# Optimization experiments

Hardware: AMD Instinct MI355X
Metric: run time of the kernel (lower is better)

## Reference

```python
import jax, jax.numpy as jnp
import numpy as np

H = 1152; NH = 16; HD = 72; INTER = 4304; DEPTH = 4
C = 3; T = 2; P = 16; G = 48; M = 2; S = G * G
MERGED = H * M * M; OUT = 2048; ROT = HD // 2  # rotary_pos_emb_dim = head_dim//2


def _ln(x, w, b, eps=1e-6):
    # manual LayerNorm decomposition (mean/var/rsqrt), fp32 like the original
    m = x.mean(-1, keepdims=True)
    xc = x - m
    v = (xc * xc).mean(-1, keepdims=True)
    return w * (xc * jax.lax.rsqrt(v + eps)) + b


def _gelu(x):
    return jax.nn.gelu(x, approximate=True)  # tanh approximation


def _rot_half(x):
    h = x.shape[-1] // 2
    return jnp.concatenate([-x[..., h:], x[..., :h]], axis=-1)


def _pos_ids():
    # Qwen merge-pattern token order: 2x2 spatial blocks are contiguous
    ids = np.arange(G * G).reshape(G // M, M, G // M, M).transpose(0, 2, 1, 3).reshape(-1)
    return jnp.asarray(ids, dtype=jnp.int32)


def setup_inputs() -> dict:
    key = jax.random.key(0)
    ks = jax.random.split(key, 16)
    w = lambda k, shape: jax.random.normal(k, shape, jnp.float32) * 0.02
    return {
        'pixel_values': jax.random.normal(ks[0], (S, C * T * P * P), jnp.float32),
        'cu_seqlens': jnp.array([0, S], jnp.int32),
        'conv_w': w(ks[1], (H, C, T, P, P)),
        'conv_b': jnp.zeros((H,), jnp.float32),
        'pos_tab': w(ks[2], (G * G, H)),
        'ln1_w': jnp.ones((DEPTH, H), jnp.float32), 'ln1_b': jnp.zeros((DEPTH, H), jnp.float32),
        'ln2_w': jnp.ones((DEPTH, H), jnp.float32), 'ln2_b': jnp.zeros((DEPTH, H), jnp.float32),
        'qkv_w': w(ks[3], (DEPTH, 3 * H, H)), 'qkv_b': jnp.zeros((DEPTH, 3 * H), jnp.float32),
        'proj_w': w(ks[4], (DEPTH, H, H)), 'proj_b': jnp.zeros((DEPTH, H), jnp.float32),
        'fc1_w': w(ks[5], (DEPTH, INTER, H)), 'fc1_b': jnp.zeros((DEPTH, INTER), jnp.float32),
        'fc2_w': w(ks[6], (DEPTH, H, INTER)), 'fc2_b': jnp.zeros((DEPTH, H), jnp.float32),
        'm_norm_w': jnp.ones((H,), jnp.float32), 'm_norm_b': jnp.zeros((H,), jnp.float32),
        'm_fc1_w': w(ks[7], (MERGED, MERGED)), 'm_fc1_b': jnp.zeros((MERGED,), jnp.float32),
        'm_fc2_w': w(ks[8], (OUT, MERGED)), 'm_fc2_b': jnp.zeros((OUT,), jnp.float32),
    }


def reference(pixel_values, cu_seqlens, conv_w, conv_b, pos_tab,
              ln1_w, ln1_b, ln2_w, ln2_b, qkv_w, qkv_b, proj_w, proj_b,
              fc1_w, fc1_b, fc2_w, fc2_b, m_norm_w, m_norm_b,
              m_fc1_w, m_fc1_b, m_fc2_w, m_fc2_b):
    pos_ids = _pos_ids()
    # Conv3d with stride == kernel over pre-extracted patches == matmul
    x = pixel_values @ conv_w.reshape(H, -1).T + conv_b            # [S, H]
    x = x + pos_tab[pos_ids]
    # 2D rotary: h-freqs and w-freqs each ROT/2 dims, concat -> ROT, dup -> HD
    inv_freq = 1.0 / (10000.0 ** (jnp.arange(0, ROT, 2, dtype=jnp.float32) / ROT))
    hp = (pos_ids // G).astype(jnp.float32)
    wp = (pos_ids % G).astype(jnp.float32)
    freqs = jnp.concatenate([hp[:, None] * inv_freq, wp[:, None] * inv_freq], axis=-1)  # [S, ROT]
    emb = jnp.concatenate([freqs, freqs], axis=-1)                 # [S, HD]
    cos = jnp.cos(emb)[:, None, :]                                 # [S, 1, HD]
    sin = jnp.sin(emb)[:, None, :]
    # varlen attention: block-diagonal mask from cu_seqlens
    seg = jnp.searchsorted(cu_seqlens, jnp.arange(S), side='right')
    mask = jnp.where(seg[:, None] == seg[None, :], 0.0, -1e9).astype(jnp.float32)
    scale = 1.0 / np.sqrt(HD)
    for i in range(DEPTH):
        h = _ln(x, ln1_w[i], ln1_b[i])
        qkv = (h @ qkv_w[i].T + qkv_b[i]).reshape(S, 3, NH, HD)
        q, k, v = qkv[:, 0], qkv[:, 1], qkv[:, 2]
        q = q * cos + _rot_half(q) * sin
        k = k * cos + _rot_half(k) * sin
        scores = jnp.einsum('qhd,khd->hqk', q, k) * scale + mask
        attn = jax.nn.softmax(scores, axis=-1)
        o = jnp.einsum('hqk,khd->qhd', attn, v).reshape(S, H)
        x = x + o @ proj_w[i].T + proj_b[i]
        h2 = _ln(x, ln2_w[i], ln2_b[i])
        x = x + _gelu(h2 @ fc1_w[i].T + fc1_b[i]) @ fc2_w[i].T + fc2_b[i]
    # patch merger: pre-merge LN -> reshape to merged -> fc1 -> gelu(tanh) -> fc2
    y = _ln(x, m_norm_w, m_norm_b).reshape(-1, MERGED)             # [S/4, MERGED]
    return _gelu(y @ m_fc1_w.T + m_fc1_b) @ m_fc2_w.T + m_fc2_b   # [S/4, OUT]
```

## Files before the change

### kernel.cpp

```cpp
#include <hip/hip_runtime.h>
#include <hip/hip_bf16.h>
#include <math.h>

#define S 2304
#define HDIM 1152
#define NHEAD 16
#define HD 72
#define INTER 4304
#define INTERP 4352
#define DEPTH 4
#define MERGED 4608
#define OUTD 2048
#define KIN 1536
#define NSPLIT 2
#define KHALF (S / NSPLIT)

typedef float f4 __attribute__((ext_vector_type(4)));
typedef short s8v __attribute__((ext_vector_type(8)));

__device__ __forceinline__ int pos_id_of(int s) {
  int a = s / 96;
  int r = s % 96;
  int b = r >> 2;
  int c = (r >> 1) & 1;
  int d = r & 1;
  return a * 96 + c * 48 + b * 2 + d;
}

__device__ __forceinline__ float gelu_f(float v) {
  const float c = 0.7978845608028654f;
  float t = tanhf(c * (v + 0.044715f * v * v * v));
  return 0.5f * v * (1.f + t);
}

__device__ __forceinline__ unsigned short f2b(float f) {
  unsigned int u = __float_as_uint(f);
  u += 0x7fffu + ((u >> 16) & 1u);
  return (unsigned short)(u >> 16);
}
__device__ __forceinline__ float b2f(unsigned short u) {
  return __uint_as_float(((unsigned int)u) << 16);
}

__device__ __forceinline__ void gload16(const void* g, void* l) {
  __builtin_amdgcn_global_load_lds(
      (const __attribute__((address_space(1))) void*)g,
      (__attribute__((address_space(3))) void*)l, 16, 0, 0);
}

__device__ __forceinline__ int xcd_swz(int flat, int nwg) {
  int q = nwg >> 3, r8 = nwg & 7;
  int xcd = flat & 7, lin = flat >> 3;
  return (xcd < r8 ? xcd * (q + 1) : r8 * (q + 1) + (xcd - r8) * q) + lin;
}

__global__ void __launch_bounds__(256) cvt_kernel(
    const float* __restrict__ src, unsigned short* __restrict__ dst,
    int N, int Ksrc, int Kdst)
{
  int idx = blockIdx.x * 256 + threadIdx.x;
  int kc = Kdst >> 3;
  if (idx >= N * kc) return;
  int r = idx / kc;
  int c8 = (idx % kc) << 3;
  const float* sp = src + (size_t)r * Ksrc + c8;
  unsigned short outv[8];
#pragma unroll
  for (int e = 0; e < 8; ++e)
    outv[e] = (c8 + e < Ksrc) ? f2b(sp[e]) : (unsigned short)0;
  *(uint4*)(dst + (size_t)r * Kdst + c8) = *(uint4*)outv;
}

__global__ void __launch_bounds__(256) gemm_bf16_kernel(
    const unsigned short* __restrict__ A, const unsigned short* __restrict__ B,
    const float* __restrict__ bias, const float* __restrict__ resid,
    void* __restrict__ Cout, int M, int Nreal, int K,
    int lda, int ldb, int ldc, int act, int outbf)
{
  __shared__ unsigned short Asm[2][128 * 32];
  __shared__ unsigned short Bsm[2][128 * 32];
  const int tid = threadIdx.x;
  const int lane = tid & 63;
  const int wv = tid >> 6;
  const int wr = wv >> 1, wc = wv & 1;

  int flat = blockIdx.y * gridDim.x + blockIdx.x;
  int swz = xcd_swz(flat, gridDim.x * gridDim.y);
  const int bm = (swz / gridDim.x) * 128;
  const int bn = (swz % gridDim.x) * 128;

  const int g8 = (lane >> 4) << 3;
  const int lr = lane & 15;

  const int srow = wv * 32 + (lane >> 2);
  const int kcol = (lane & 3) << 3;
  int ar0 = bm + srow;      if (ar0 >= M) ar0 = M - 1;
  int ar1 = bm + srow + 16; if (ar1 >= M) ar1 = M - 1;
  int br0 = bn + srow;      if (br0 >= Nreal) br0 = Nreal - 1;
  int br1 = bn + srow + 16; if (br1 >= Nreal) br1 = Nreal - 1;
  const unsigned short* Ag0 = A + (size_t)ar0 * lda + kcol;
  const unsigned short* Ag1 = A + (size_t)ar1 * lda + kcol;
  const unsigned short* Bg0 = B + (size_t)br0 * ldb + kcol;
  const unsigned short* Bg1 = B + (size_t)br1 * ldb + kcol;

  f4 acc[4][4];
#pragma unroll
  for (int m = 0; m < 4; ++m)
#pragma unroll
    for (int n = 0; n < 4; ++n) { acc[m][n].x = 0.f; acc[m][n].y = 0.f; acc[m][n].z = 0.f; acc[m][n].w = 0.f; }

  const int nt = K >> 5;
  gload16(Ag0, &Asm[0][(wv * 32) * 32]);
  gload16(Ag1, &Asm[0][(wv * 32 + 16) * 32]);
  gload16(Bg0, &Bsm[0][(wv * 32) * 32]);
  gload16(Bg1, &Bsm[0][(wv * 32 + 16) * 32]);
  asm volatile("s_waitcnt vmcnt(0)" ::: "memory");
  __syncthreads();

  int cur = 0;
  for (int t = 0; t < nt; ++t) {
    if (t + 1 < nt) {
      int ko = (t + 1) << 5;
      gload16(Ag0 + ko, &Asm[cur ^ 1][(wv * 32) * 32]);
      gload16(Ag1 + ko, &Asm[cur ^ 1][(wv * 32 + 16) * 32]);
      gload16(Bg0 + ko, &Bsm[cur ^ 1][(wv * 32) * 32]);
      gload16(Bg1 + ko, &Bsm[cur ^ 1][(wv * 32 + 16) * 32]);
    }
    s8v af[4], bf[4];
#pragma unroll
    for (int m = 0; m < 4; ++m)
      af[m] = *(const s8v*)&Asm[cur][(wr * 64 + m * 16 + lr) * 32 + g8];
#pragma unroll
    for (int n = 0; n < 4; ++n)
      bf[n] = *(const s8v*)&Bsm[cur][(wc * 64 + n * 16 + lr) * 32 + g8];
#pragma unroll
    for (int m = 0; m < 4; ++m)
#pragma unroll
      for (int n = 0; n < 4; ++n)
        acc[m][n] = __builtin_amdgcn_mfma_f32_16x16x32_bf16(af[m], bf[n], acc[m][n], 0, 0, 0);
    asm volatile("s_waitcnt vmcnt(0)" ::: "memory");
    __syncthreads();
    cur ^= 1;
  }

  const int g4 = (lane >> 4) << 2;
#pragma unroll
  for (int m = 0; m < 4; ++m) {
    int r = bm + wr * 64 + m * 16 + g4;
#pragma unroll
    for (int n = 0; n < 4; ++n) {
      int cidx = bn + wc * 64 + n * 16 + lr;
      float bb = (cidx < Nreal) ? bias[cidx] : 0.f;
#pragma unroll
      for (int j = 0; j < 4; ++j) {
        int rr = r + j;
        if (rr < M) {
          float v = acc[m][n][j] + bb;
          if (act) v = gelu_f(v);
          if (cidx >= Nreal) v = 0.f;
          if (resid) v += resid[(size_t)rr * ldc + cidx];
          if (outbf) ((unsigned short*)Cout)[(size_t)rr * ldc + cidx] = f2b(v);
          else       ((float*)Cout)[(size_t)rr * ldc + cidx] = v;
        }
      }
    }
  }
}

__global__ void __launch_bounds__(256) gemm_bf16_splitk_kernel(
    const unsigned short* __restrict__ A, const unsigned short* __restrict__ B,
    float* __restrict__ Cpart, int M, int N, int Kc, int lda, int ldb)
{
  __shared__ unsigned short Asm[2][128 * 32];
  __shared__ unsigned short Bsm[2][128 * 32];
  const int tid = threadIdx.x;
  const int lane = tid & 63;
  const int wv = tid >> 6;
  const int wr = wv >> 1, wc = wv & 1;

  int flat = blockIdx.y * gridDim.x + blockIdx.x;
  int swz = xcd_swz(flat, gridDim.x * gridDim.y);
  const int bm = (swz / gridDim.x) * 128;
  const int bn = (swz % gridDim.x) * 128;
  const int z = blockIdx.z;
  const int kbase = z * Kc;

  const int g8 = (lane >> 4) << 3;
  const int lr = lane & 15;

  const int srow = wv * 32 + (lane >> 2);
  const int kcol = (lane & 3) << 3;
  int ar0 = bm + srow;      if (ar0 >= M) ar0 = M - 1;
  int ar1 = bm + srow + 16; if (ar1 >= M) ar1 = M - 1;
  int br0 = bn + srow;      if (br0 >= N) br0 = N - 1;
  int br1 = bn + srow + 16; if (br1 >= N) br1 = N - 1;
  const unsigned short* Ag0 = A + (size_t)ar0 * lda + kbase + kcol;
  const unsigned short* Ag1 = A + (size_t)ar1 * lda + kbase + kcol;
  const unsigned short* Bg0 = B + (size_t)br0 * ldb + kbase + kcol;
  const unsigned short* Bg1 = B + (size_t)br1 * ldb + kbase + kcol;

  f4 acc[4][4];
#pragma unroll
  for (int m = 0; m < 4; ++m)
#pragma unroll
    for (int n = 0; n < 4; ++n) { acc[m][n].x = 0.f; acc[m][n].y = 0.f; acc[m][n].z = 0.f; acc[m][n].w = 0.f; }

  const int nt = Kc >> 5;
  gload16(Ag0, &Asm[0][(wv * 32) * 32]);
  gload16(Ag1, &Asm[0][(wv * 32 + 16) * 32]);
  gload16(Bg0, &Bsm[0][(wv * 32) * 32]);
  gload16(Bg1, &Bsm[0][(wv * 32 + 16) * 32]);
  asm volatile("s_waitcnt vmcnt(0)" ::: "memory");
  __syncthreads();

  int cur = 0;
  for (int t = 0; t < nt; ++t) {
    if (t + 1 < nt) {
      int ko = (t + 1) << 5;
      gload16(Ag0 + ko, &Asm[cur ^ 1][(wv * 32) * 32]);
      gload16(Ag1 + ko, &Asm[cur ^ 1][(wv * 32 + 16) * 32]);
      gload16(Bg0 + ko, &Bsm[cur ^ 1][(wv * 32) * 32]);
      gload16(Bg1 + ko, &Bsm[cur ^ 1][(wv * 32 + 16) * 32]);
    }
    s8v af[4], bf[4];
#pragma unroll
    for (int m = 0; m < 4; ++m)
      af[m] = *(const s8v*)&Asm[cur][(wr * 64 + m * 16 + lr) * 32 + g8];
#pragma unroll
    for (int n = 0; n < 4; ++n)
      bf[n] = *(const s8v*)&Bsm[cur][(wc * 64 + n * 16 + lr) * 32 + g8];
#pragma unroll
    for (int m = 0; m < 4; ++m)
#pragma unroll
      for (int n = 0; n < 4; ++n)
        acc[m][n] = __builtin_amdgcn_mfma_f32_16x16x32_bf16(af[m], bf[n], acc[m][n], 0, 0, 0);
    asm volatile("s_waitcnt vmcnt(0)" ::: "memory");
    __syncthreads();
    cur ^= 1;
  }

  float* Cz = Cpart + (size_t)z * M * N;
  const int g4 = (lane >> 4) << 2;
#pragma unroll
  for (int m = 0; m < 4; ++m) {
    int r = bm + wr * 64 + m * 16 + g4;
#pragma unroll
    for (int n = 0; n < 4; ++n) {
      int cidx = bn + wc * 64 + n * 16 + lr;
      if (cidx < N) {
#pragma unroll
        for (int j = 0; j < 4; ++j) {
          int rr = r + j;
          if (rr < M) Cz[(size_t)rr * N + cidx] = acc[m][n][j];
        }
      }
    }
  }
}

__global__ void __launch_bounds__(256) combine_gemm_kernel(
    const float* __restrict__ Cpart, int nz, const float* __restrict__ bias,
    const float* __restrict__ resid, float* __restrict__ out, int M, int N)
{
  int idx = blockIdx.x * 256 + threadIdx.x;
  int total = (M * N) >> 2;
  if (idx >= total) return;
  int r = idx / (N >> 2);
  int c4 = (idx % (N >> 2)) << 2;
  size_t off = (size_t)r * N + c4;
  float4 s = *(const float4*)(Cpart + off);
  for (int z = 1; z < nz; ++z) {
    float4 p = *(const float4*)(Cpart + (size_t)z * M * N + off);
    s.x += p.x; s.y += p.y; s.z += p.z; s.w += p.w;
  }
  float4 b = *(const float4*)(bias + c4);
  s.x += b.x; s.y += b.y; s.z += b.z; s.w += b.w;
  if (resid) {
    float4 rv = *(const float4*)(resid + off);
    s.x += rv.x; s.y += rv.y; s.z += rv.z; s.w += rv.w;
  }
  *(float4*)(out + off) = s;
}

__global__ void __launch_bounds__(256) ln_kernel(const float* __restrict__ xin,
    const float* __restrict__ w, const float* __restrict__ b, unsigned short* __restrict__ out)
{
  __shared__ float red[8];
  const int row = blockIdx.x;
  const float* xr = xin + (size_t)row * HDIM;
  float s = 0.f;
  for (int i = threadIdx.x; i < HDIM; i += 256) s += xr[i];
#pragma unroll
  for (int off = 32; off > 0; off >>= 1) s += __shfl_down(s, off);
  if ((threadIdx.x & 63) == 0) red[threadIdx.x >> 6] = s;
  __syncthreads();
  float mean = (red[0] + red[1] + red[2] + red[3]) * (1.f / HDIM);
  float s2 = 0.f;
  for (int i = threadIdx.x; i < HDIM; i += 256) { float d = xr[i] - mean; s2 += d * d; }
#pragma unroll
  for (int off = 32; off > 0; off >>= 1) s2 += __shfl_down(s2, off);
  __syncthreads();
  if ((threadIdx.x & 63) == 0) red[threadIdx.x >> 6] = s2;
  __syncthreads();
  float var = (red[0] + red[1] + red[2] + red[3]) * (1.f / HDIM);
  float rstd = rsqrtf(var + 1e-6f);
  for (int i = threadIdx.x; i < HDIM; i += 256)
    out[(size_t)row * HDIM + i] = f2b(w[i] * ((xr[i] - mean) * rstd) + b[i]);
}

__global__ void __launch_bounds__(256) add_pos_kernel(float* __restrict__ x, const float* __restrict__ pos_tab)
{
  int s = blockIdx.x;
  int pid = pos_id_of(s);
  const float* pr = pos_tab + (size_t)pid * HDIM;
  float* xr = x + (size_t)s * HDIM;
  for (int i = threadIdx.x; i < HDIM; i += 256) xr[i] += pr[i];
}

__global__ void rope_tables_kernel(float* __restrict__ cosT, float* __restrict__ sinT)
{
  int s = blockIdx.x;
  int j = threadIdx.x;
  if (j >= 36) return;
  int pid = pos_id_of(s);
  float hp = (float)(pid / 48);
  float wp = (float)(pid % 48);
  int f = (j < 18) ? j : (j - 18);
  float inv = powf(10000.f, -(2.f * (float)f) / 36.f);
  float ang = ((j < 18) ? hp : wp) * inv;
  cosT[s * 36 + j] = cosf(ang);
  sinT[s * 36 + j] = sinf(ang);
}

__global__ void seg_kernel(const int* __restrict__ cu, int n_cu, int* __restrict__ seg)
{
  int i = blockIdx.x * 256 + threadIdx.x;
  if (i >= S) return;
  int s = 0;
  for (int t = 0; t < n_cu; ++t) s += (cu[t] <= i) ? 1 : 0;
  seg[i] = s;
}

__global__ void __launch_bounds__(256) rope_kernel(unsigned short* __restrict__ qkv,
    const float* __restrict__ cosT, const float* __restrict__ sinT)
{
  int idx = blockIdx.x * 256 + threadIdx.x;
  int d = idx % 36; int t = idx / 36;
  int hh = t % NHEAD; t /= NHEAD;
  int qk = t & 1; int s = t >> 1;
  unsigned short* base = qkv + (size_t)s * 3456 + qk * 1152 + hh * 72;
  float c = cosT[s * 36 + d], sn = sinT[s * 36 + d];
  float x0 = b2f(base[d]), x1 = b2f(base[d + 36]);
  base[d] = f2b(x0 * c - x1 * sn);
  base[d + 36] = f2b(x1 * c + x0 * sn);
}

#define KT 64
#define KSL 88
#define ASCALE 0.11785113019775793f

__global__ void __launch_bounds__(256) flash_mfma_kernel(
    const unsigned short* __restrict__ qkv, unsigned short* __restrict__ opart,
    float* __restrict__ ml, const int* __restrict__ seg)
{
  __shared__ __align__(16) unsigned short Ks[64 * KSL];
  __shared__ __align__(16) unsigned short Vt[80 * 72];
  __shared__ __align__(16) unsigned short Ps[4][16 * 72];

  const int tid = threadIdx.x;
  const int lane = tid & 63;
  const int wv = tid >> 6;
  const int g = lane >> 4;
  const int c = lane & 15;

  int flat = (blockIdx.z * NHEAD + blockIdx.y) * (S / 64) + blockIdx.x;
  int swz = xcd_swz(flat, (S / 64) * NHEAD * NSPLIT);
  const int q0 = (swz % (S / 64)) * 64;
  const int hh = (swz / (S / 64)) % NHEAD;
  const int sidx = swz / ((S / 64) * NHEAD);
  const int kbeg = sidx * KHALF;

  for (int i = tid; i < 64 * 8; i += 256) {
    int r = i >> 3, cc = i & 7;
    *(unsigned int*)&Ks[r * KSL + 72 + cc * 2] = 0u;
  }
  for (int i = tid; i < 288; i += 256)
    *(unsigned int*)&Vt[72 * 72 + i * 2] = 0u;

  s8v qf[3];
  {
    const int qrow = q0 + wv * 16 + c;
    const unsigned short* qb = qkv + (size_t)qrow * 3456 + hh * HD;
#pragma unroll
    for (int ks = 0; ks < 3; ++ks) {
      int k = ks * 32 + g * 8;
      if (k <= 64) qf[ks] = *(const s8v*)(qb + k);
      else {
        s8v z;
#pragma unroll
        for (int t = 0; t < 8; ++t) z[t] = 0;
        qf[ks] = z;
      }
    }
  }

  int msg[4];
#pragma unroll
  for (int j = 0; j < 4; ++j) msg[j] = seg[q0 + wv * 16 + g * 4 + j];

  float mj[4], lj[4];
#pragma unroll
  for (int j = 0; j < 4; ++j) { mj[j] = -1e30f; lj[j] = 0.f; }
  f4 acco[5];
#pragma unroll
  for (int n = 0; n < 5; ++n) { acco[n].x = 0.f; acco[n].y = 0.f; acco[n].z = 0.f; acco[n].w = 0.f; }

  uint4 kreg[3], vreg[3];

#define STAGE_LOAD(KT0)                                                                  \
  {                                                                                      \
    _Pragma("unroll")                                                                    \
    for (int ii = 0; ii < 3; ++ii) {                                                     \
      int idx = tid + ii * 256;                                                          \
      if (idx < 576) {                                                                   \
        int rK = idx / 9, cK = idx % 9;                                                  \
        kreg[ii] = *(const uint4*)(qkv + (size_t)((KT0) + rK) * 3456 + 1152 + hh * HD + cK * 8); \
        int rV = idx & 63, cV = idx >> 6;                                                \
        vreg[ii] = *(const uint4*)(qkv + (size_t)((KT0) + rV) * 3456 + 2304 + hh * HD + cV * 8); \
      }                                                                                  \
    }                                                                                    \
  }

#define STAGE_WRITE()                                                                    \
  {                                                                                      \
    _Pragma("unroll")                                                                    \
    for (int ii = 0; ii < 3; ++ii) {                                                     \
      int idx = tid + ii * 256;                                                          \
      if (idx < 576) {                                                                   \
        int rK = idx / 9, cK = idx % 9;                                                  \
        *(uint4*)&Ks[rK * KSL + cK * 8] = kreg[ii];                                      \
        int rV = idx & 63, cV = idx >> 6;                                                \
        unsigned short vv[8];                                                            \
        *(uint4*)vv = vreg[ii];                                                          \
        _Pragma("unroll")                                                                \
        for (int e = 0; e < 8; ++e) Vt[(cV * 8 + e) * 72 + rV] = vv[e];                  \
      }                                                                                  \
    }                                                                                    \
  }

  STAGE_LOAD(kbeg);
  asm volatile("s_waitcnt vmcnt(0)" ::: "memory");
  STAGE_WRITE();
  asm volatile("s_waitcnt lgkmcnt(0)" ::: "memory");
  __builtin_amdgcn_s_barrier();
  __builtin_amdgcn_sched_barrier(0);

  for (int k0 = kbeg; k0 < kbeg + KHALF; k0 += KT) {
    const bool more = (k0 + KT < kbeg + KHALF);
    if (more) STAGE_LOAD(k0 + KT);

    int sgn[4];
#pragma unroll
    for (int n = 0; n < 4; ++n) sgn[n] = seg[k0 + n * 16 + c];

    f4 accs[4];
#pragma unroll
    for (int n = 0; n < 4; ++n) { accs[n].x = 0.f; accs[n].y = 0.f; accs[n].z = 0.f; accs[n].w = 0.f; }
#pragma unroll
    for (int ks = 0; ks < 3; ++ks) {
      const int koff = (ks < 2) ? (ks * 32 + g * 8) : 64;
#pragma unroll
      for (int n = 0; n < 4; ++n) {
        s8v bk = *(const s8v*)&Ks[(n * 16 + c) * KSL + koff];
        accs[n] = __builtin_amdgcn_mfma_f32_16x16x32_bf16(qf[ks], bk, accs[n], 0, 0, 0);
      }
    }

    float sc[4][4], mx[4];
#pragma unroll
    for (int j = 0; j < 4; ++j) mx[j] = -1e30f;
#pragma unroll
    for (int n = 0; n < 4; ++n)
#pragma unroll
      for (int j = 0; j < 4; ++j) {
        float v = accs[n][j] * ASCALE + ((sgn[n] == msg[j]) ? 0.f : -1e9f);
        sc[n][j] = v;
        mx[j] = fmaxf(mx[j], v);
      }
#pragma unroll
    for (int j = 0; j < 4; ++j) {
      mx[j] = fmaxf(mx[j], __shfl_xor(mx[j], 1));
      mx[j] = fmaxf(mx[j], __shfl_xor(mx[j], 2));
      mx[j] = fmaxf(mx[j], __shfl_xor(mx[j], 4));
      mx[j] = fmaxf(mx[j], __shfl_xor(mx[j], 8));
    }
    float alpha[4], rs[4];
#pragma unroll
    for (int j = 0; j < 4; ++j) {
      float mn = fmaxf(mj[j], mx[j]);
      alpha[j] = __expf(mj[j] - mn);
      mj[j] = mn;
      rs[j] = 0.f;
    }
    float pv[4][4];
#pragma unroll
    for (int n = 0; n < 4; ++n)
#pragma unroll
      for (int j = 0; j < 4; ++j) {
        float p = __expf(sc[n][j] - mj[j]);
        pv[n][j] = p;
        rs[j] += p;
      }
#pragma unroll
    for (int j = 0; j < 4; ++j) {
      rs[j] += __shfl_xor(rs[j], 1);
      rs[j] += __shfl_xor(rs[j], 2);
      rs[j] += __shfl_xor(rs[j], 4);
      rs[j] += __shfl_xor(rs[j], 8);
      lj[j] = lj[j] * alpha[j] + rs[j];
    }
#pragma unroll
    for (int n = 0; n < 4; ++n)
#pragma unroll
      for (int j = 0; j < 4; ++j)
        Ps[wv][(g * 4 + j) * 72 + n * 16 + c] = f2b(pv[n][j]);

#pragma unroll
    for (int n = 0; n < 5; ++n)
#pragma unroll
      for (int j = 0; j < 4; ++j) acco[n][j] *= alpha[j];

    asm volatile("s_waitcnt lgkmcnt(0)" ::: "memory");
    __builtin_amdgcn_sched_barrier(0);

#pragma unroll
    for (int ks = 0; ks < 2; ++ks) {
      s8v pa = *(const s8v*)&Ps[wv][c * 72 + ks * 32 + g * 8];
#pragma unroll
      for (int n = 0; n < 5; ++n) {
        s8v vb = *(const s8v*)&Vt[(n * 16 + c) * 72 + ks * 32 + g * 8];
        acco[n] = __builtin_amdgcn_mfma_f32_16x16x32_bf16(pa, vb, acco[n], 0, 0, 0);
      }
    }

    asm volatile("s_waitcnt lgkmcnt(0)" ::: "memory");
    __builtin_amdgcn_s_barrier();
    if (more) {
      asm volatile("s_waitcnt vmcnt(0)" ::: "memory");
      STAGE_WRITE();
      asm volatile("s_waitcnt lgkmcnt(0)" ::: "memory");
    }
    __builtin_amdgcn_s_barrier();
    __builtin_amdgcn_sched_barrier(0);
  }

  unsigned short* op = opart + (size_t)(sidx * NHEAD + hh) * S * 72;
#pragma unroll
  for (int n = 0; n < 5; ++n) {
    int col = n * 16 + c;
    if (col < HD) {
#pragma unroll
      for (int j = 0; j < 4; ++j) {
        int row = q0 + wv * 16 + g * 4 + j;
        op[(size_t)row * 72 + col] = f2b(acco[n][j]);
      }
    }
  }
  if (c == 0) {
#pragma unroll
    for (int j = 0; j < 4; ++j) {
      int row = q0 + wv * 16 + g * 4 + j;
      float2 v; v.x = mj[j]; v.y = lj[j];
      *(float2*)&ml[((size_t)(sidx * NHEAD + hh) * S + row) * 2] = v;
    }
  }
}

__global__ void __launch_bounds__(256) attn_combine_kernel(
    const unsigned short* __restrict__ opart, const float* __restrict__ ml,
    unsigned short* __restrict__ oout)
{
  int idx = blockIdx.x * 256 + threadIdx.x;
  int d = idx % 72;
  int row = (idx / 72) % S;
  int hh = idx / (72 * S);
  size_t b1 = (size_t)hh * S + row;
  size_t b2 = (size_t)(NHEAD + hh) * S + row;
  float m1 = ml[b1 * 2], l1 = ml[b1 * 2 + 1];
  float m2 = ml[b2 * 2], l2 = ml[b2 * 2 + 1];
  float ms = fmaxf(m1, m2);
  float a1 = __expf(m1 - ms), a2 = __expf(m2 - ms);
  float l = a1 * l1 + a2 * l2;
  float o = (a1 * b2f(opart[b1 * 72 + d]) + a2 * b2f(opart[b2 * 72 + d])) / l;
  oout[(size_t)row * HDIM + hh * 72 + d] = f2b(o);
}

extern "C" void kernel_launch(void* const* d_in, const int* in_sizes, int n_in,
                              void* d_out, int out_size, void* d_ws, size_t ws_size,
                              hipStream_t stream)
{
  (void)n_in; (void)out_size; (void)ws_size;
  const float* pix    = (const float*)d_in[0];
  const int*   cu     = (const int*)d_in[1];
  const int    n_cu   = in_sizes[1];
  const float* conv_w = (const float*)d_in[2];
  const float* conv_b = (const float*)d_in[3];
  const float* pos_tab= (const float*)d_in[4];
  const float* ln1_w  = (const float*)d_in[5];
  const float* ln1_b  = (const float*)d_in[6];
  const float* ln2_w  = (const float*)d_in[7];
  const float* ln2_b  = (const float*)d_in[8];
  const float* qkv_w  = (const float*)d_in[9];
  const float* qkv_b  = (const float*)d_in[10];
  const float* proj_w = (const float*)d_in[11];
  const float* proj_b = (const float*)d_in[12];
  const float* fc1_w  = (const float*)d_in[13];
  const float* fc1_b  = (const float*)d_in[14];
  const float* fc2_w  = (const float*)d_in[15];
  const float* fc2_b  = (const float*)d_in[16];
  const float* mn_w   = (const float*)d_in[17];
  const float* mn_b   = (const float*)d_in[18];
  const float* mf1_w  = (const float*)d_in[19];
  const float* mf1_b  = (const float*)d_in[20];
  const float* mf2_w  = (const float*)d_in[21];
  const float* mf2_b  = (const float*)d_in[22];
  float* out = (float*)d_out;

  float*    x      = (float*)d_ws;
  unsigned short* h_bf   = (unsigned short*)(x + (size_t)S * HDIM);
  unsigned short* qkv_bf = h_bf + (size_t)S * HDIM;
  unsigned short* A_bf   = qkv_bf + (size_t)S * 3456;
  unsigned short* Wbuf   = A_bf + (size_t)S * INTERP;
  float*    cosT   = (float*)(Wbuf + (size_t)MERGED * MERGED);
  float*    sinT   = cosT + (size_t)S * 36;
  int*      seg    = (int*)(sinT + (size_t)S * 36);
  unsigned short* pix_bf = A_bf;
  unsigned short* opart  = A_bf;
  float*    ml     = (float*)(A_bf + (size_t)NSPLIT * NHEAD * S * 72);
  float*    part_h = (float*)h_bf;
  float*    part_q = (float*)qkv_bf;

  auto cvt = [&](const float* src, unsigned short* dst, int N, int Ksrc, int Kdst) {
    int total = N * (Kdst >> 3);
    cvt_kernel<<<(total + 255) / 256, 256, 0, stream>>>(src, dst, N, Ksrc, Kdst);
  };
  auto gemm = [&](const unsigned short* A, const unsigned short* B, const float* bias,
                  const float* resid, void* C, int M, int N, int K,
                  int lda, int ldb, int ldc, int act, int outbf) {
    gemm_bf16_kernel<<<dim3((N + 127) / 128, (M + 127) / 128), 256, 0, stream>>>(
        A, B, bias, resid, C, M, N, K, lda, ldb, ldc, act, outbf);
  };
  auto gemm_sk = [&](const unsigned short* A, const unsigned short* B, float* part,
                     const float* bias, const float* resid, float* C,
                     int M, int N, int K, int nz, int lda, int ldb) {
    gemm_bf16_splitk_kernel<<<dim3(N / 128, (M + 127) / 128, nz), 256, 0, stream>>>(
        A, B, part, M, N, K / nz, lda, ldb);
    combine_gemm_kernel<<<((M * N / 4) + 255) / 256, 256, 0, stream>>>(
        part, nz, bias, resid, C, M, N);
  };

  cvt(pix, pix_bf, S, KIN, KIN);
  cvt(conv_w, Wbuf, HDIM, KIN, KIN);
  gemm_sk(pix_bf, Wbuf, part_h, conv_b, nullptr, x, S, HDIM, KIN, 2, KIN, KIN);
  add_pos_kernel<<<S, 256, 0, stream>>>(x, pos_tab);
  rope_tables_kernel<<<S, 64, 0, stream>>>(cosT, sinT);
  seg_kernel<<<(S + 255) / 256, 256, 0, stream>>>(cu, n_cu, seg);

  for (int layer = 0; layer < DEPTH; ++layer) {
    ln_kernel<<<S, 256, 0, stream>>>(x, ln1_w + layer * HDIM, ln1_b + layer * HDIM, h_bf);
    cvt(qkv_w + (size_t)layer * 3456 * HDIM, Wbuf, 3456, HDIM, HDIM);
    gemm(h_bf, Wbuf, qkv_b + layer * 3456, nullptr, qkv_bf, S, 3456, HDIM, HDIM, HDIM, 3456, 0, 1);
    rope_kernel<<<(S * 2 * NHEAD * 36) / 256, 256, 0, stream>>>(qkv_bf, cosT, sinT);
    flash_mfma_kernel<<<dim3(S / 64, NHEAD, NSPLIT), 256, 0, stream>>>(qkv_bf, opart, ml, seg);
    attn_combine_kernel<<<(NHEAD * S * 72) / 256, 256, 0, stream>>>(opart, ml, h_bf);
    cvt(proj_w + (size_t)layer * HDIM * HDIM, Wbuf, HDIM, HDIM, HDIM);
    gemm_sk(h_bf, Wbuf, part_q, proj_b + layer * HDIM, x, x, S, HDIM, HDIM, 3, HDIM, HDIM);
    ln_kernel<<<S, 256, 0, stream>>>(x, ln2_w + layer * HDIM, ln2_b + layer * HDIM, h_bf);
    cvt(fc1_w + (size_t)layer * INTER * HDIM, Wbuf, INTER, HDIM, HDIM);
    gemm(h_bf, Wbuf, fc1_b + layer * INTER, nullptr, A_bf, S, INTER, HDIM, HDIM, HDIM, INTERP, 1, 1);
    cvt(fc2_w + (size_t)layer * HDIM * INTER, Wbuf, HDIM, INTER, INTERP);
    gemm_sk(A_bf, Wbuf, part_h, fc2_b + layer * HDIM, x, x, S, HDIM, INTERP, 2, INTERP, INTERP);
  }

  ln_kernel<<<S, 256, 0, stream>>>(x, mn_w, mn_b, h_bf);
  cvt(mf1_w, Wbuf, MERGED, MERGED, MERGED);
  gemm(h_bf, Wbuf, mf1_b, nullptr, A_bf, 576, MERGED, MERGED, MERGED, MERGED, MERGED, 1, 1);
  cvt(mf2_w, Wbuf, OUTD, MERGED, MERGED);
  gemm_sk(A_bf, Wbuf, part_h, mf2_b, nullptr, out, 576, OUTD, MERGED, 4, MERGED, MERGED);
}
```

Baseline: 1.879 ms.

## Fuse split-K combine with LayerNorm, use 64-row GEMM tiles, widen attention split

Split-K partial-sum combine, bias, residual and positional add are fused into the LayerNorm kernel, which also writes the residual stream. The standalone LN and add_pos launches and one full pass over x go away. The full GEMM moves to a 64x128 tile for more blocks. Flash attention now handles 128 query rows per block as two 16-row sub-blocks per wave, skips per-element mask lookups when a tile lies in one segment, and splits keys four ways with a generalized combine. The trade-offs are more partial output traffic from the wider split and lower per-block reuse from the smaller GEMM tile.

```diff
diff --git a/kernel.cpp b/kernel.cpp
--- a/kernel.cpp
+++ b/kernel.cpp
@@ -12,7 +12,7 @@
 #define MERGED 4608
 #define OUTD 2048
 #define KIN 1536
-#define NSPLIT 2
+#define NSPLIT 4
 #define KHALF (S / NSPLIT)
 
 typedef float f4 __attribute__((ext_vector_type(4)));
@@ -71,49 +71,43 @@
   *(uint4*)(dst + (size_t)r * Kdst + c8) = *(uint4*)outv;
 }
 
-__global__ void __launch_bounds__(256) gemm_bf16_kernel(
+__global__ void __launch_bounds__(256) gemm_bf16_m64_kernel(
     const unsigned short* __restrict__ A, const unsigned short* __restrict__ B,
-    const float* __restrict__ bias, const float* __restrict__ resid,
-    void* __restrict__ Cout, int M, int Nreal, int K,
-    int lda, int ldb, int ldc, int act, int outbf)
-{
-  __shared__ unsigned short Asm[2][128 * 32];
+    const float* __restrict__ bias, void* __restrict__ Cout,
+    int M, int Nreal, int K, int lda, int ldb, int ldc, int act, int outbf)
+{
+  __shared__ unsigned short Asm[2][64 * 32];
   __shared__ unsigned short Bsm[2][128 * 32];
   const int tid = threadIdx.x;
   const int lane = tid & 63;
   const int wv = tid >> 6;
-  const int wr = wv >> 1, wc = wv & 1;
 
   int flat = blockIdx.y * gridDim.x + blockIdx.x;
   int swz = xcd_swz(flat, gridDim.x * gridDim.y);
-  const int bm = (swz / gridDim.x) * 128;
+  const int bm = (swz / gridDim.x) * 64;
   const int bn = (swz % gridDim.x) * 128;
 
   const int g8 = (lane >> 4) << 3;
   const int lr = lane & 15;
 
-  const int srow = wv * 32 + (lane >> 2);
-  const int kcol = (lane & 3) << 3;
-  int ar0 = bm + srow;      if (ar0 >= M) ar0 = M - 1;
-  int ar1 = bm + srow + 16; if (ar1 >= M) ar1 = M - 1;
-  int br0 = bn + srow;      if (br0 >= Nreal) br0 = Nreal - 1;
-  int br1 = bn + srow + 16; if (br1 >= Nreal) br1 = Nreal - 1;
-  const unsigned short* Ag0 = A + (size_t)ar0 * lda + kcol;
-  const unsigned short* Ag1 = A + (size_t)ar1 * lda + kcol;
-  const unsigned short* Bg0 = B + (size_t)br0 * ldb + kcol;
-  const unsigned short* Bg1 = B + (size_t)br1 * ldb + kcol;
-
-  f4 acc[4][4];
+  const int lrow = lane >> 2;
+  const int kq = (lane & 3) << 3;
+  const unsigned short* AgP = A + (size_t)(bm + wv * 16 + lrow) * lda + kq;
+  int brow1 = bn + wv * 16 + lrow;      if (brow1 >= Nreal) brow1 = Nreal - 1;
+  int brow2 = bn + 64 + wv * 16 + lrow; if (brow2 >= Nreal) brow2 = Nreal - 1;
+  const unsigned short* BgP1 = B + (size_t)brow1 * ldb + kq;
+  const unsigned short* BgP2 = B + (size_t)brow2 * ldb + kq;
+
+  f4 acc[4][2];
 #pragma unroll
   for (int m = 0; m < 4; ++m)
 #pragma unroll
-    for (int n = 0; n < 4; ++n) { acc[m][n].x = 0.f; acc[m][n].y = 0.f; acc[m][n].z = 0.f; acc[m][n].w = 0.f; }
+    for (int n = 0; n < 2; ++n) { acc[m][n].x = 0.f; acc[m][n].y = 0.f; acc[m][n].z = 0.f; acc[m][n].w = 0.f; }
 
   const int nt = K >> 5;
-  gload16(Ag0, &Asm[0][(wv * 32) * 32]);
-  gload16(Ag1, &Asm[0][(wv * 32 + 16) * 32]);
-  gload16(Bg0, &Bsm[0][(wv * 32) * 32]);
-  gload16(Bg1, &Bsm[0][(wv * 32 + 16) * 32]);
+  gload16(AgP, &Asm[0][(wv * 16) * 32]);
+  gload16(BgP1, &Bsm[0][(wv * 16) * 32]);
+  gload16(BgP2, &Bsm[0][(64 + wv * 16) * 32]);
   asm volatile("s_waitcnt vmcnt(0)" ::: "memory");
   __syncthreads();
 
@@ -121,22 +115,21 @@
   for (int t = 0; t < nt; ++t) {
     if (t + 1 < nt) {
       int ko = (t + 1) << 5;
-      gload16(Ag0 + ko, &Asm[cur ^ 1][(wv * 32) * 32]);
-      gload16(Ag1 + ko, &Asm[cur ^ 1][(wv * 32 + 16) * 32]);
-      gload16(Bg0 + ko, &Bsm[cur ^ 1][(wv * 32) * 32]);
-      gload16(Bg1 + ko, &Bsm[cur ^ 1][(wv * 32 + 16) * 32]);
-    }
-    s8v af[4], bf[4];
+      gload16(AgP + ko, &Asm[cur ^ 1][(wv * 16) * 32]);
+      gload16(BgP1 + ko, &Bsm[cur ^ 1][(wv * 16) * 32]);
+      gload16(BgP2 + ko, &Bsm[cur ^ 1][(64 + wv * 16) * 32]);
+    }
+    s8v af[4], bf[2];
 #pragma unroll
     for (int m = 0; m < 4; ++m)
-      af[m] = *(const s8v*)&Asm[cur][(wr * 64 + m * 16 + lr) * 32 + g8];
-#pragma unroll
-    for (int n = 0; n < 4; ++n)
-      bf[n] = *(const s8v*)&Bsm[cur][(wc * 64 + n * 16 + lr) * 32 + g8];
+      af[m] = *(const s8v*)&Asm[cur][(m * 16 + lr) * 32 + g8];
+#pragma unroll
+    for (int n = 0; n < 2; ++n)
+      bf[n] = *(const s8v*)&Bsm[cur][(wv * 32 + n * 16 + lr) * 32 + g8];
 #pragma unroll
     for (int m = 0; m < 4; ++m)
 #pragma unroll
-      for (int n = 0; n < 4; ++n)
+      for (int n = 0; n < 2; ++n)
         acc[m][n] = __builtin_amdgcn_mfma_f32_16x16x32_bf16(af[m], bf[n], acc[m][n], 0, 0, 0);
     asm volatile("s_waitcnt vmcnt(0)" ::: "memory");
     __syncthreads();
@@ -146,22 +139,19 @@
   const int g4 = (lane >> 4) << 2;
 #pragma unroll
   for (int m = 0; m < 4; ++m) {
-    int r = bm + wr * 64 + m * 16 + g4;
-#pragma unroll
-    for (int n = 0; n < 4; ++n) {
-      int cidx = bn + wc * 64 + n * 16 + lr;
+    int r = bm + m * 16 + g4;
+#pragma unroll
+    for (int n = 0; n < 2; ++n) {
+      int cidx = bn + wv * 32 + n * 16 + lr;
       float bb = (cidx < Nreal) ? bias[cidx] : 0.f;
 #pragma unroll
       for (int j = 0; j < 4; ++j) {
         int rr = r + j;
-        if (rr < M) {
-          float v = acc[m][n][j] + bb;
-          if (act) v = gelu_f(v);
-          if (cidx >= Nreal) v = 0.f;
-          if (resid) v += resid[(size_t)rr * ldc + cidx];
-          if (outbf) ((unsigned short*)Cout)[(size_t)rr * ldc + cidx] = f2b(v);
-          else       ((float*)Cout)[(size_t)rr * ldc + cidx] = v;
-        }
+        float v = acc[m][n][j] + bb;
+        if (act) v = gelu_f(v);
+        if (cidx >= Nreal) v = 0.f;
+        if (outbf) ((unsigned short*)Cout)[(size_t)rr * ldc + cidx] = f2b(v);
+        else       ((float*)Cout)[(size_t)rr * ldc + cidx] = v;
       }
     }
   }
@@ -282,39 +272,58 @@
   *(float4*)(out + off) = s;
 }
 
-__global__ void __launch_bounds__(256) ln_kernel(const float* __restrict__ xin,
-    const float* __restrict__ w, const float* __restrict__ b, unsigned short* __restrict__ out)
+__global__ void __launch_bounds__(256) combine_ln_kernel(
+    const float* __restrict__ Cpart, int nz, const float* __restrict__ bias,
+    const float* __restrict__ resid, const float* __restrict__ pos_tab,
+    float* __restrict__ xout, const float* __restrict__ lnw,
+    const float* __restrict__ lnb, unsigned short* __restrict__ hout)
 {
   __shared__ float red[8];
   const int row = blockIdx.x;
-  const float* xr = xin + (size_t)row * HDIM;
-  float s = 0.f;
-  for (int i = threadIdx.x; i < HDIM; i += 256) s += xr[i];
-#pragma unroll
-  for (int off = 32; off > 0; off >>= 1) s += __shfl_down(s, off);
-  if ((threadIdx.x & 63) == 0) red[threadIdx.x >> 6] = s;
+  const int tid = threadIdx.x;
+  const float* pos = pos_tab ? pos_tab + (size_t)pos_id_of(row) * HDIM : nullptr;
+  float v[5];
+  float s1 = 0.f;
+#pragma unroll
+  for (int t = 0; t < 5; ++t) {
+    int i = tid + t * 256;
+    float s = 0.f;
+    if (i < HDIM) {
+      size_t off = (size_t)row * HDIM + i;
+      s = Cpart[off];
+      for (int z = 1; z < nz; ++z) s += Cpart[(size_t)z * ((size_t)S * HDIM) + off];
+      s += bias[i];
+      if (resid) s += resid[off];
+      if (pos) s += pos[i];
+      xout[off] = s;
+    }
+    v[t] = s;
+    s1 += s;
+  }
+#pragma unroll
+  for (int off = 32; off > 0; off >>= 1) s1 += __shfl_down(s1, off);
+  if ((tid & 63) == 0) red[tid >> 6] = s1;
   __syncthreads();
   float mean = (red[0] + red[1] + red[2] + red[3]) * (1.f / HDIM);
   float s2 = 0.f;
-  for (int i = threadIdx.x; i < HDIM; i += 256) { float d = xr[i] - mean; s2 += d * d; }
+#pragma unroll
+  for (int t = 0; t < 5; ++t) {
+    int i = tid + t * 256;
+    if (i < HDIM) { float d = v[t] - mean; s2 += d * d; }
+  }
 #pragma unroll
   for (int off = 32; off > 0; off >>= 1) s2 += __shfl_down(s2, off);
   __syncthreads();
-  if ((threadIdx.x & 63) == 0) red[threadIdx.x >> 6] = s2;
+  if ((tid & 63) == 0) red[tid >> 6] = s2;
   __syncthreads();
   float var = (red[0] + red[1] + red[2] + red[3]) * (1.f / HDIM);
   float rstd = rsqrtf(var + 1e-6f);
-  for (int i = threadIdx.x; i < HDIM; i += 256)
-    out[(size_t)row * HDIM + i] = f2b(w[i] * ((xr[i] - mean) * rstd) + b[i]);
-}
-
-__global__ void __launch_bounds__(256) add_pos_kernel(float* __restrict__ x, const float* __restrict__ pos_tab)
-{
-  int s = blockIdx.x;
-  int pid = pos_id_of(s);
-  const float* pr = pos_tab + (size_t)pid * HDIM;
-  float* xr = x + (size_t)s * HDIM;
-  for (int i = threadIdx.x; i < HDIM; i += 256) xr[i] += pr[i];
+#pragma unroll
+  for (int t = 0; t < 5; ++t) {
+    int i = tid + t * 256;
+    if (i < HDIM)
+      hout[(size_t)row * HDIM + i] = f2b(lnw[i] * ((v[t] - mean) * rstd) + lnb[i]);
+  }
 }
 
 __global__ void rope_tables_kernel(float* __restrict__ cosT, float* __restrict__ sinT)
@@ -373,12 +382,13 @@
   const int g = lane >> 4;
   const int c = lane & 15;
 
-  int flat = (blockIdx.z * NHEAD + blockIdx.y) * (S / 64) + blockIdx.x;
-  int swz = xcd_swz(flat, (S / 64) * NHEAD * NSPLIT);
-  const int q0 = (swz % (S / 64)) * 64;
-  const int hh = (swz / (S / 64)) % NHEAD;
-  const int sidx = swz / ((S / 64) * NHEAD);
+  int flat = (blockIdx.z * NHEAD + blockIdx.y) * (S / 128) + blockIdx.x;
+  int swz = xcd_swz(flat, (S / 128) * NHEAD * NSPLIT);
+  const int q0 = (swz % (S / 128)) * 128;
+  const int hh = (swz / (S / 128)) % NHEAD;
+  const int sidx = swz / ((S / 128) * NHEAD);
   const int kbeg = sidx * KHALF;
+  const int qr = q0 + wv * 32;
 
   for (int i = tid; i < 64 * 8; i += 256) {
     int r = i >> 3, cc = i & 7;
@@ -387,33 +397,35 @@
   for (int i = tid; i < 288; i += 256)
     *(unsigned int*)&Vt[72 * 72 + i * 2] = 0u;
 
-  s8v qf[3];
+  const bool uni = (seg[q0] == seg[q0 + 127]) && (seg[kbeg] == seg[kbeg + KHALF - 1])
+                && (seg[q0] == seg[kbeg]);
+  const int msgA = seg[qr + c];
+  const int msgB = seg[qr + 16 + c];
+
+  s8v qfA[3], qfB[3];
   {
-    const int qrow = q0 + wv * 16 + c;
-    const unsigned short* qb = qkv + (size_t)qrow * 3456 + hh * HD;
+    const unsigned short* qa = qkv + (size_t)(qr + c) * 3456 + hh * HD;
+    const unsigned short* qb = qkv + (size_t)(qr + 16 + c) * 3456 + hh * HD;
 #pragma unroll
     for (int ks = 0; ks < 3; ++ks) {
       int k = ks * 32 + g * 8;
-      if (k <= 64) qf[ks] = *(const s8v*)(qb + k);
+      if (k <= 64) { qfA[ks] = *(const s8v*)(qa + k); qfB[ks] = *(const s8v*)(qb + k); }
       else {
         s8v z;
 #pragma unroll
         for (int t = 0; t < 8; ++t) z[t] = 0;
-        qf[ks] = z;
+        qfA[ks] = z; qfB[ks] = z;
       }
     }
   }
 
-  int msg[4];
-#pragma unroll
-  for (int j = 0; j < 4; ++j) msg[j] = seg[q0 + wv * 16 + g * 4 + j];
-
-  float mj[4], lj[4];
-#pragma unroll
-  for (int j = 0; j < 4; ++j) { mj[j] = -1e30f; lj[j] = 0.f; }
-  f4 acco[5];
-#pragma unroll
-  for (int n = 0; n < 5; ++n) { acco[n].x = 0.f; acco[n].y = 0.f; acco[n].z = 0.f; acco[n].w = 0.f; }
+  float mA = -1e30f, lA = 0.f, mB = -1e30f, lB = 0.f;
+  f4 accoA[5], accoB[5];
+#pragma unroll
+  for (int n = 0; n < 5; ++n) {
+    accoA[n].x = 0.f; accoA[n].y = 0.f; accoA[n].z = 0.f; accoA[n].w = 0.f;
+    accoB[n].x = 0.f; accoB[n].y = 0.f; accoB[n].z = 0.f; accoB[n].w = 0.f;
+  }
 
   uint4 kreg[3], vreg[3];
 
@@ -448,6 +460,85 @@
     }                                                                                    \
   }
 
+#define SUBBLOCK(QF, MSG, MM, LL, ACCO, ROWOFF)                                          \
+  {                                                                                      \
+    f4 accs[4];                                                                          \
+    _Pragma("unroll")                                                                    \
+    for (int nk = 0; nk < 4; ++nk) { accs[nk].x = 0.f; accs[nk].y = 0.f; accs[nk].z = 0.f; accs[nk].w = 0.f; } \
+    _Pragma("unroll")                                                                    \
+    for (int ks = 0; ks < 3; ++ks) {                                                     \
+      const int koff = (ks < 2) ? (ks * 32 + g * 8) : 64;                                \
+      _Pragma("unroll")                                                                  \
+      for (int nk = 0; nk < 4; ++nk) {                                                   \
+        s8v bk = *(const s8v*)&Ks[(nk * 16 + c) * KSL + koff];                           \
+        accs[nk] = __builtin_amdgcn_mfma_f32_16x16x32_bf16(bk, QF[ks], accs[nk], 0, 0, 0); \
+      }                                                                                  \
+    }                                                                                    \
+    float sc[4][4];                                                                      \
+    float mx = -1e30f;                                                                   \
+    if (uni) {                                                                           \
+      _Pragma("unroll")                                                                  \
+      for (int nk = 0; nk < 4; ++nk)                                                     \
+        _Pragma("unroll")                                                                \
+        for (int j = 0; j < 4; ++j) {                                                    \
+          float vv = accs[nk][j] * ASCALE;                                               \
+          sc[nk][j] = vv; mx = fmaxf(mx, vv);                                            \
+        }                                                                                \
+    } else {                                                                             \
+      _Pragma("unroll")                                                                  \
+      for (int nk = 0; nk < 4; ++nk)                                                     \
+        _Pragma("unroll")                                                                \
+        for (int j = 0; j < 4; ++j) {                                                    \
+          int kk = k0 + nk * 16 + g * 4 + j;                                             \
+          float vv = accs[nk][j] * ASCALE + ((seg[kk] == MSG) ? 0.f : -1e9f);             \
+          sc[nk][j] = vv; mx = fmaxf(mx, vv);                                            \
+        }                                                                                \
+    }                                                                                    \
+    mx = fmaxf(mx, __shfl_xor(mx, 16));                                                  \
+    mx = fmaxf(mx, __shfl_xor(mx, 32));                                                  \
+    float mn = fmaxf(MM, mx);                                                            \
+    float al = __expf(MM - mn);                                                          \
+    MM = mn;                                                                             \
+    float rsum = 0.f;                                                                    \
+    float p[4][4];                                                                       \
+    _Pragma("unroll")                                                                    \
+    for (int nk = 0; nk < 4; ++nk)                                                       \
+      _Pragma("unroll")                                                                  \
+      for (int j = 0; j < 4; ++j) {                                                      \
+        float pv = __expf(sc[nk][j] - mn);                                               \
+        p[nk][j] = pv; rsum += pv;                                                       \
+      }                                                                                  \
+    rsum += __shfl_xor(rsum, 16);                                                        \
+    rsum += __shfl_xor(rsum, 32);                                                        \
+    LL = LL * al + rsum;                                                                 \
+    _Pragma("unroll")                                                                    \
+    for (int nk = 0; nk < 4; ++nk) {                                                     \
+      unsigned int w0 = (unsigned int)f2b(p[nk][0]) | ((unsigned int)f2b(p[nk][1]) << 16); \
+      unsigned int w1 = (unsigned int)f2b(p[nk][2]) | ((unsigned int)f2b(p[nk][3]) << 16); \
+      uint2 wv2; wv2.x = w0; wv2.y = w1;                                                 \
+      *(uint2*)&Ps[wv][c * 72 + nk * 16 + g * 4] = wv2;                                  \
+    }                                                                                    \
+    float alpha_row[4];                                                                  \
+    _Pragma("unroll")                                                                    \
+    for (int j = 0; j < 4; ++j)                                                          \
+      alpha_row[j] = __shfl(al, (lane & 48) | (g * 4 + j));                              \
+    _Pragma("unroll")                                                                    \
+    for (int n = 0; n < 5; ++n)                                                          \
+      _Pragma("unroll")                                                                  \
+      for (int j = 0; j < 4; ++j) ACCO[n][j] *= alpha_row[j];                            \
+    asm volatile("s_waitcnt lgkmcnt(0)" ::: "memory");                                   \
+    __builtin_amdgcn_sched_barrier(0);                                                   \
+    _Pragma("unroll")                                                                    \
+    for (int ks = 0; ks < 2; ++ks) {                                                     \
+      s8v pa = *(const s8v*)&Ps[wv][c * 72 + ks * 32 + g * 8];                           \
+      _Pragma("unroll")                                                                  \
+      for (int n = 0; n < 5; ++n) {                                                      \
+        s8v vb = *(const s8v*)&Vt[(n * 16 + c) * 72 + ks * 32 + g * 8];                  \
+        ACCO[n] = __builtin_amdgcn_mfma_f32_16x16x32_bf16(pa, vb, ACCO[n], 0, 0, 0);     \
+      }                                                                                  \
+    }                                                                                    \
+  }
+
   STAGE_LOAD(kbeg);
   asm volatile("s_waitcnt vmcnt(0)" ::: "memory");
   STAGE_WRITE();
@@ -459,89 +550,8 @@
     const bool more = (k0 + KT < kbeg + KHALF);
     if (more) STAGE_LOAD(k0 + KT);
 
-    int sgn[4];
-#pragma unroll
-    for (int n = 0; n < 4; ++n) sgn[n] = seg[k0 + n * 16 + c];
-
-    f4 accs[4];
-#pragma unroll
-    for (int n = 0; n < 4; ++n) { accs[n].x = 0.f; accs[n].y = 0.f; accs[n].z = 0.f; accs[n].w = 0.f; }
-#pragma unroll
-    for (int ks = 0; ks < 3; ++ks) {
-      const int koff = (ks < 2) ? (ks * 32 + g * 8) : 64;
-#pragma unroll
-      for (int n = 0; n < 4; ++n) {
-        s8v bk = *(const s8v*)&Ks[(n * 16 + c) * KSL + koff];
-        accs[n] = __builtin_amdgcn_mfma_f32_16x16x32_bf16(qf[ks], bk, accs[n], 0, 0, 0);
-      }
-    }
-
-    float sc[4][4], mx[4];
-#pragma unroll
-    for (int j = 0; j < 4; ++j) mx[j] = -1e30f;
-#pragma unroll
-    for (int n = 0; n < 4; ++n)
-#pragma unroll
-      for (int j = 0; j < 4; ++j) {
-        float v = accs[n][j] * ASCALE + ((sgn[n] == msg[j]) ? 0.f : -1e9f);
-        sc[n][j] = v;
-        mx[j] = fmaxf(mx[j], v);
-      }
-#pragma unroll
-    for (int j = 0; j < 4; ++j) {
-      mx[j] = fmaxf(mx[j], __shfl_xor(mx[j], 1));
-      mx[j] = fmaxf(mx[j], __shfl_xor(mx[j], 2));
-      mx[j] = fmaxf(mx[j], __shfl_xor(mx[j], 4));
-      mx[j] = fmaxf(mx[j], __shfl_xor(mx[j], 8));
-    }
-    float alpha[4], rs[4];
-#pragma unroll
-    for (int j = 0; j < 4; ++j) {
-      float mn = fmaxf(mj[j], mx[j]);
-      alpha[j] = __expf(mj[j] - mn);
-      mj[j] = mn;
-      rs[j] = 0.f;
-    }
-    float pv[4][4];
-#pragma unroll
-    for (int n = 0; n < 4; ++n)
-#pragma unroll
-      for (int j = 0; j < 4; ++j) {
-        float p = __expf(sc[n][j] - mj[j]);
-        pv[n][j] = p;
-        rs[j] += p;
-      }
-#pragma unroll
-    for (int j = 0; j < 4; ++j) {
-      rs[j] += __shfl_xor(rs[j], 1);
-      rs[j] += __shfl_xor(rs[j], 2);
-      rs[j] += __shfl_xor(rs[j], 4);
-      rs[j] += __shfl_xor(rs[j], 8);
-      lj[j] = lj[j] * alpha[j] + rs[j];
-    }
-#pragma unroll
-    for (int n = 0; n < 4; ++n)
-#pragma unroll
-      for (int j = 0; j < 4; ++j)
-        Ps[wv][(g * 4 + j) * 72 + n * 16 + c] = f2b(pv[n][j]);
-
-#pragma unroll
-    for (int n = 0; n < 5; ++n)
-#pragma unroll
-      for (int j = 0; j < 4; ++j) acco[n][j] *= alpha[j];
-
-    asm volatile("s_waitcnt lgkmcnt(0)" ::: "memory");
-    __builtin_amdgcn_sched_barrier(0);
-
-#pragma unroll
-    for (int ks = 0; ks < 2; ++ks) {
-      s8v pa = *(const s8v*)&Ps[wv][c * 72 + ks * 32 + g * 8];
-#pragma unroll
-      for (int n = 0; n < 5; ++n) {
-        s8v vb = *(const s8v*)&Vt[(n * 16 + c) * 72 + ks * 32 + g * 8];
-        acco[n] = __builtin_amdgcn_mfma_f32_16x16x32_bf16(pa, vb, acco[n], 0, 0, 0);
-      }
-    }
+    SUBBLOCK(qfA, msgA, mA, lA, accoA, 0);
+    SUBBLOCK(qfB, msgB, mB, lB, accoB, 16);
 
     asm volatile("s_waitcnt lgkmcnt(0)" ::: "memory");
     __builtin_amdgcn_s_barrier();
@@ -555,23 +565,33 @@
   }
 
   unsigned short* op = opart + (size_t)(sidx * NHEAD + hh) * S * 72;
+  float lrA[4], mrA[4], lrB[4], mrB[4];
+#pragma unroll
+  for (int j = 0; j < 4; ++j) {
+    int src = (lane & 48) | (g * 4 + j);
+    lrA[j] = __shfl(lA, src); mrA[j] = __shfl(mA, src);
+    lrB[j] = __shfl(lB, src); mrB[j] = __shfl(mB, src);
+  }
 #pragma unroll
   for (int n = 0; n < 5; ++n) {
     int col = n * 16 + c;
     if (col < HD) {
 #pragma unroll
       for (int j = 0; j < 4; ++j) {
-        int row = q0 + wv * 16 + g * 4 + j;
-        op[(size_t)row * 72 + col] = f2b(acco[n][j]);
+        int rowA = qr + g * 4 + j;
+        op[(size_t)rowA * 72 + col] = f2b(accoA[n][j]);
+        op[(size_t)(rowA + 16) * 72 + col] = f2b(accoB[n][j]);
       }
     }
   }
   if (c == 0) {
 #pragma unroll
     for (int j = 0; j < 4; ++j) {
-      int row = q0 + wv * 16 + g * 4 + j;
-      float2 v; v.x = mj[j]; v.y = lj[j];
-      *(float2*)&ml[((size_t)(sidx * NHEAD + hh) * S + row) * 2] = v;
+      int rowA = qr + g * 4 + j;
+      float2 va; va.x = mrA[j]; va.y = lrA[j];
+      *(float2*)&ml[((size_t)(sidx * NHEAD + hh) * S + rowA) * 2] = va;
+      float2 vb; vb.x = mrB[j]; vb.y = lrB[j];
+      *(float2*)&ml[((size_t)(sidx * NHEAD + hh) * S + rowA + 16) * 2] = vb;
     }
   }
 }
@@ -584,15 +604,23 @@
   int d = idx % 72;
   int row = (idx / 72) % S;
   int hh = idx / (72 * S);
-  size_t b1 = (size_t)hh * S + row;
-  size_t b2 = (size_t)(NHEAD + hh) * S + row;
-  float m1 = ml[b1 * 2], l1 = ml[b1 * 2 + 1];
-  float m2 = ml[b2 * 2], l2 = ml[b2 * 2 + 1];
-  float ms = fmaxf(m1, m2);
-  float a1 = __expf(m1 - ms), a2 = __expf(m2 - ms);
-  float l = a1 * l1 + a2 * l2;
-  float o = (a1 * b2f(opart[b1 * 72 + d]) + a2 * b2f(opart[b2 * 72 + d])) / l;
-  oout[(size_t)row * HDIM + hh * 72 + d] = f2b(o);
+  float mv[NSPLIT], lv[NSPLIT];
+  float ms = -1e30f;
+#pragma unroll
+  for (int z = 0; z < NSPLIT; ++z) {
+    size_t b = (size_t)(z * NHEAD + hh) * S + row;
+    mv[z] = ml[b * 2]; lv[z] = ml[b * 2 + 1];
+    ms = fmaxf(ms, mv[z]);
+  }
+  float l = 0.f, o = 0.f;
+#pragma unroll
+  for (int z = 0; z < NSPLIT; ++z) {
+    size_t b = (size_t)(z * NHEAD + hh) * S + row;
+    float a = __expf(mv[z] - ms);
+    l += a * lv[z];
+    o += a * b2f(opart[b * 72 + d]);
+  }
+  oout[(size_t)row * HDIM + hh * 72 + d] = f2b(o / l);
 }
 
 extern "C" void kernel_launch(void* const* d_in, const int* in_sizes, int n_in,
@@ -644,47 +672,53 @@
     int total = N * (Kdst >> 3);
     cvt_kernel<<<(total + 255) / 256, 256, 0, stream>>>(src, dst, N, Ksrc, Kdst);
   };
-  auto gemm = [&](const unsigned short* A, const unsigned short* B, const float* bias,
-                  const float* resid, void* C, int M, int N, int K,
-                  int lda, int ldb, int ldc, int act, int outbf) {
-    gemm_bf16_kernel<<<dim3((N + 127) / 128, (M + 127) / 128), 256, 0, stream>>>(
-        A, B, bias, resid, C, M, N, K, lda, ldb, ldc, act, outbf);
+  auto gemm64 = [&](const unsigned short* A, const unsigned short* B, const float* bias,
+                    void* C, int M, int N, int K, int lda, int ldb, int ldc, int act, int outbf) {
+    gemm_bf16_m64_kernel<<<dim3((N + 127) / 128, M / 64), 256, 0, stream>>>(
+        A, B, bias, C, M, N, K, lda, ldb, ldc, act, outbf);
   };
-  auto gemm_sk = [&](const unsigned short* A, const unsigned short* B, float* part,
-                     const float* bias, const float* resid, float* C,
-                     int M, int N, int K, int nz, int lda, int ldb) {
+  auto splitk = [&](const unsigned short* A, const unsigned short* B, float* part,
+                    int M, int N, int K, int nz, int lda, int ldb) {
     gemm_bf16_splitk_kernel<<<dim3(N / 128, (M + 127) / 128, nz), 256, 0, stream>>>(
         A, B, part, M, N, K / nz, lda, ldb);
-    combine_gemm_kernel<<<((M * N / 4) + 255) / 256, 256, 0, stream>>>(
-        part, nz, bias, resid, C, M, N);
+  };
+  auto comb_ln = [&](float* part, int nz, const float* bias, const float* resid,
+                     const float* pos, const float* lw, const float* lb) {
+    combine_ln_kernel<<<S, 256, 0, stream>>>(part, nz, bias, resid, pos, x, lw, lb, h_bf);
   };
 
   cvt(pix, pix_bf, S, KIN, KIN);
   cvt(conv_w, Wbuf, HDIM, KIN, KIN);
-  gemm_sk(pix_bf, Wbuf, part_h, conv_b, nullptr, x, S, HDIM, KIN, 2, KIN, KIN);
-  add_pos_kernel<<<S, 256, 0, stream>>>(x, pos_tab);
+  splitk(pix_bf, Wbuf, part_h, S, HDIM, KIN, 2, KIN, KIN);
   rope_tables_kernel<<<S, 64, 0, stream>>>(cosT, sinT);
   seg_kernel<<<(S + 255) / 256, 256, 0, stream>>>(cu, n_cu, seg);
+  comb_ln(part_h, 2, conv_b, nullptr, pos_tab, ln1_w, ln1_b);
 
   for (int layer = 0; layer < DEPTH; ++layer) {
-    ln_kernel<<<S, 256, 0, stream>>>(x, ln1_w + layer * HDIM, ln1_b + layer * HDIM, h_bf);
     cvt(qkv_w + (size_t)layer * 3456 * HDIM, Wbuf, 3456, HDIM, HDIM);
-    gemm(h_bf, Wbuf, qkv_b + layer * 3456, nullptr, qkv_bf, S, 3456, HDIM, HDIM, HDIM, 3456, 0, 1);
+    gemm64(h_bf, Wbuf, qkv_b + layer * 3456, qkv_bf, S, 3456, HDIM, HDIM, HDIM, 3456, 0, 1);
     rope_kernel<<<(S * 2 * NHEAD * 36) / 256, 256, 0, stream>>>(qkv_bf, cosT, sinT);
-    flash_mfma_kernel<<<dim3(S / 64, NHEAD, NSPLIT), 256, 0, stream>>>(qkv_bf, opart, ml, seg);
+    flash_mfma_kernel<<<dim3(S / 128, NHEAD, NSPLIT), 256, 0, stream>>>(qkv_bf, opart, ml, seg);
     attn_combine_kernel<<<(NHEAD * S * 72) / 256, 256, 0, stream>>>(opart, ml, h_bf);
     cvt(proj_w + (size_t)layer * HDIM * HDIM, Wbuf, HDIM, HDIM, HDIM);
-    gemm_sk(h_bf, Wbuf, part_q, proj_b + layer * HDIM, x, x, S, HDIM, HDIM, 3, HDIM, HDIM);
-    ln_kernel<<<S, 256, 0, stream>>>(x, ln2_w + layer * HDIM, ln2_b + layer * HDIM, h_bf);
+    splitk(h_bf, Wbuf, part_q, S, HDIM, HDIM, 3, HDIM, HDIM);
+    comb_ln(part_q, 3, proj_b + layer * HDIM, x, nullptr,
+            ln2_w + layer * HDIM, ln2_b + layer * HDIM);
     cvt(fc1_w + (size_t)layer * INTER * HDIM, Wbuf, INTER, HDIM, HDIM);
-    gemm(h_bf, Wbuf, fc1_b + layer * INTER, nullptr, A_bf, S, INTER, HDIM, HDIM, HDIM, INTERP, 1, 1);
+    gemm64(h_bf, Wbuf, fc1_b + layer * INTER, A_bf, S, INTER, HDIM, HDIM, HDIM, INTERP, 1, 1);
     cvt(fc2_w + (size_t)layer * HDIM * INTER, Wbuf, HDIM, INTER, INTERP);
-    gemm_sk(A_bf, Wbuf, part_h, fc2_b + layer * HDIM, x, x, S, HDIM, INTERP, 2, INTERP, INTERP);
-  }
-
-  ln_kernel<<<S, 256, 0, stream>>>(x, mn_w, mn_b, h_bf);
+    splitk(A_bf, Wbuf, part_h, S, HDIM, INTERP, 2, INTERP, INTERP);
+    if (layer < DEPTH - 1)
+      comb_ln(part_h, 2, fc2_b + layer * HDIM, x, nullptr,
+              ln1_w + (layer + 1) * HDIM, ln1_b + (layer + 1) * HDIM);
+    else
+      comb_ln(part_h, 2, fc2_b + layer * HDIM, x, nullptr, mn_w, mn_b);
+  }
+
   cvt(mf1_w, Wbuf, MERGED, MERGED, MERGED);
-  gemm(h_bf, Wbuf, mf1_b, nullptr, A_bf, 576, MERGED, MERGED, MERGED, MERGED, MERGED, 1, 1);
+  gemm64(h_bf, Wbuf, mf1_b, A_bf, 576, MERGED, MERGED, MERGED, MERGED, MERGED, 1, 1);
   cvt(mf2_w, Wbuf, OUTD, MERGED, MERGED);
-  gemm_sk(A_bf, Wbuf, part_h, mf2_b, nullptr, out, 576, OUTD, MERGED, 4, MERGED, MERGED);
-}
+  splitk(A_bf, Wbuf, part_h, 576, OUTD, MERGED, 4, MERGED, MERGED);
+  combine_gemm_kernel<<<((576 * OUTD / 4) + 255) / 256, 256, 0, stream>>>(
+      part_h, 4, mf2_b, nullptr, out, 576, OUTD);
+}
```

New measurement: 1.741 ms. -7.3%, faster.
